# Kernel tuning notes

Hardware: AMD Instinct MI355X
Metric: run time of the kernel (lower is better)

## Reference

```python
import jax, jax.numpy as jnp
import numpy as np

H = 8
D_MODEL = 1024
DIM_G = 64
WAVE_LEN = 1000.0


def box_relational_embedding(f_g):
    # f_g: [B, N, 4] -> [B, N, N, 64] trigonometric geometry embedding
    B, N, _ = f_g.shape
    x_min, y_min, x_max, y_max = jnp.split(f_g, 4, axis=-1)  # each [B, N, 1]
    cx = (x_min + x_max) * 0.5
    cy = (y_min + y_max) * 0.5
    w = x_max - x_min + 1.0
    h = y_max - y_min + 1.0
    # row i vs column j deltas, normalized by row box size
    dx = jnp.log(jnp.maximum(jnp.abs((cx - cx.reshape(B, 1, N)) / w), 1e-3))
    dy = jnp.log(jnp.maximum(jnp.abs((cy - cy.reshape(B, 1, N)) / h), 1e-3))
    dw = jnp.log(w / w.reshape(B, 1, N))
    dh = jnp.log(h / h.reshape(B, 1, N))
    pos = jnp.stack([dx, dy, dw, dh], axis=-1)  # [B, N, N, 4]
    feat_range = jnp.arange(DIM_G // 8, dtype=jnp.float32) / (DIM_G / 8.0)
    dim_mat = 1.0 / jnp.power(WAVE_LEN, feat_range)  # [8]
    mul = (100.0 * pos)[..., None] * dim_mat  # [B, N, N, 4, 8]
    mul = mul.reshape(B, N, N, DIM_G // 2)
    return jnp.concatenate([jnp.sin(mul), jnp.cos(mul)], axis=-1)  # [B, N, N, 64]


def setup_inputs() -> dict:
    key = jax.random.key(0)
    ks = jax.random.split(key, 12)
    B, N, D = 16, 256, D_MODEL
    q = jax.random.normal(ks[0], (B, N, D), jnp.float32)
    k = jax.random.normal(ks[1], (B, N, D), jnp.float32)
    v = jax.random.normal(ks[2], (B, N, D), jnp.float32)
    # valid boxes: x_max > x_min, y_max > y_min
    xy = jax.random.uniform(ks[3], (B, N, 2), jnp.float32) * 100.0
    wh = jax.random.uniform(ks[4], (B, N, 2), jnp.float32) * 50.0 + 1.0
    input_box = jnp.concatenate([xy, xy + wh], axis=-1)  # [B, N, 4]
    s = 0.02
    Wq = jax.random.normal(ks[5], (D, D), jnp.float32) * s
    Wk = jax.random.normal(ks[6], (D, D), jnp.float32) * s
    Wv = jax.random.normal(ks[7], (D, D), jnp.float32) * s
    Wo = jax.random.normal(ks[8], (D, D), jnp.float32) * s
    bq = jnp.zeros((D,), jnp.float32)
    bk = jnp.zeros((D,), jnp.float32)
    bv = jnp.zeros((D,), jnp.float32)
    bo = jnp.zeros((D,), jnp.float32)
    Wg = jax.random.normal(ks[9], (H, DIM_G), jnp.float32) * 0.1  # stacked per-head Linear(64,1)
    bg = jax.random.normal(ks[10], (H,), jnp.float32) * 0.1
    return {"input_query": q, "input_key": k, "input_value": v, "input_box": input_box,
            "Wq": Wq, "bq": bq, "Wk": Wk, "bk": bk, "Wv": Wv, "bv": bv,
            "Wg": Wg, "bg": bg, "Wo": Wo, "bo": bo}


def reference(input_query, input_key, input_value, input_box,
              Wq, bq, Wk, bk, Wv, bv, Wg, bg, Wo, bo):
    B, N, D = input_query.shape
    d_k = D // H

    def proj(x, W, b):
        return (x @ W + b).reshape(B, N, H, d_k).transpose(0, 2, 1, 3)  # [B,H,N,dk]

    q = proj(input_query, Wq, bq)
    k = proj(input_key, Wk, bk)
    v = proj(input_value, Wv, bv)

    emb = box_relational_embedding(input_box)  # [B, N, N, 64]
    # per-head Linear(64 -> 1), stacked: [B, H, N, N]
    rel_w = jax.nn.relu(jnp.einsum('bmng,hg->bhmn', emb, Wg) + bg[None, :, None, None])

    scores = jnp.einsum('bhqd,bhkd->bhqk', q, k) / np.sqrt(d_k).astype(np.float32)
    logits = jnp.log(jnp.maximum(rel_w, 1e-6)) + scores
    attn = jax.nn.softmax(logits, axis=-1)  # [B, H, N, N]
    out = jnp.einsum('bhqk,bhkd->bhqd', attn, v)
    out = out.transpose(0, 2, 1, 3).reshape(B, N, D)
    return out @ Wo + bo
```

## Files before the change

kernel.cpp:

```cpp
#include <hip/hip_runtime.h>
#include <hip/hip_bf16.h>
#include <math.h>

#define B_  16
#define N_  256
#define D_  1024
#define H_  8
#define DK_ 128

typedef unsigned short u16;
typedef __attribute__((ext_vector_type(8))) short s8v;
typedef __attribute__((ext_vector_type(4))) float f4v;

__device__ __forceinline__ u16 f2b(float x) {
    union { float f; unsigned u; } v; v.f = x;
    unsigned r = v.u + 0x7fffu + ((v.u >> 16) & 1u);
    return (u16)(r >> 16);
}

__device__ __forceinline__ void gload16(void* lds, const void* g) {
    __builtin_amdgcn_global_load_lds(
        (const __attribute__((address_space(1))) void*)g,
        (__attribute__((address_space(3))) void*)lds, 16, 0, 0);
}

__global__ __launch_bounds__(256)
void cvt_kernel(const float* __restrict__ x0, const float* __restrict__ x1,
                const float* __restrict__ x2, u16* __restrict__ out)
{
    const float* in = (blockIdx.y == 0) ? x0 : (blockIdx.y == 1) ? x1 : x2;
    u16* o = out + (size_t)blockIdx.y * 4194304;
    const int i = blockIdx.x * 256 + threadIdx.x;
    const float4 a = ((const float4*)in)[2 * i];
    const float4 b = ((const float4*)in)[2 * i + 1];
    union { u16 s[8]; uint4 v; } t;
    t.s[0] = f2b(a.x); t.s[1] = f2b(a.y); t.s[2] = f2b(a.z); t.s[3] = f2b(a.w);
    t.s[4] = f2b(b.x); t.s[5] = f2b(b.y); t.s[6] = f2b(b.z); t.s[7] = f2b(b.w);
    ((uint4*)o)[i] = t.v;
}

__global__ __launch_bounds__(256)
void cvtT_kernel(const float* __restrict__ W0, const float* __restrict__ W1,
                 const float* __restrict__ W2, const float* __restrict__ W3,
                 u16* __restrict__ out)
{
    const float* W = (blockIdx.z == 0) ? W0 : (blockIdx.z == 1) ? W1 :
                     (blockIdx.z == 2) ? W2 : W3;
    u16* o = out + (size_t)blockIdx.z * (D_ * D_);
    __shared__ float t[32][33];
    const int k0 = blockIdx.x * 32, n0 = blockIdx.y * 32;
    const int c = threadIdx.x & 31, r8 = threadIdx.x >> 5;
#pragma unroll
    for (int rr = 0; rr < 4; ++rr)
        t[r8 + rr * 8][c] = W[(size_t)(k0 + r8 + rr * 8) * D_ + n0 + c];
    __syncthreads();
#pragma unroll
    for (int rr = 0; rr < 4; ++rr)
        o[(size_t)(n0 + r8 + rr * 8) * D_ + k0 + c] = f2b(t[c][r8 + rr * 8]);
}

__global__ __launch_bounds__(256)
void gemm_kernel(const u16* __restrict__ A0, const u16* __restrict__ Wt0,
                 const float* __restrict__ b0, const float* __restrict__ b1,
                 const float* __restrict__ b2, void* __restrict__ outb,
                 int mode)
{
    __shared__ __align__(16) u16 As[128][32];
    __shared__ __align__(16) u16 Bs[128][32];

    const int z = blockIdx.z;
    const u16* A  = A0  + (size_t)z * 4194304;
    const u16* Wt = Wt0 + (size_t)z * 1048576;
    const float* bias = (z == 0) ? b0 : (z == 1) ? b1 : b2;

    const int bid = blockIdx.x;
    const int xcd = bid & 7;
    const int wic = bid >> 3;
    const int by  = xcd * 4 + (wic & 3);
    const int bx  = wic >> 2;
    const int m0  = by * 128;
    const int n0  = bx * 128;

    const int tid  = threadIdx.x;
    const int lane = tid & 63;
    const int w    = tid >> 6;
    const int l15  = lane & 15;
    const int l4   = lane >> 4;
    const int wr   = w >> 1;
    const int wc   = w & 1;

    const int gr = tid >> 2;
    const int gc = (tid & 3) * 8;
    const u16* asrc = A  + (size_t)(m0 + gr) * 1024 + gc;
    const u16* bsrc = Wt + (size_t)(n0 + gr) * 1024 + gc;

    f4v acc[4][4] = {};

    for (int kt = 0; kt < 32; ++kt) {
        const int k0 = kt * 32;
        __syncthreads();
        gload16(&As[gr][gc],      asrc + k0);
        gload16(&As[64 + gr][gc], asrc + 64 * 1024 + k0);
        gload16(&Bs[gr][gc],      bsrc + k0);
        gload16(&Bs[64 + gr][gc], bsrc + 64 * 1024 + k0);
        __syncthreads();

        s8v af[4], bf[4];
#pragma unroll
        for (int i = 0; i < 4; ++i)
            af[i] = *(const s8v*)&As[wr * 64 + i * 16 + l15][l4 * 8];
#pragma unroll
        for (int j = 0; j < 4; ++j)
            bf[j] = *(const s8v*)&Bs[wc * 64 + j * 16 + l15][l4 * 8];
#pragma unroll
        for (int i = 0; i < 4; ++i)
#pragma unroll
            for (int j = 0; j < 4; ++j)
                acc[i][j] = __builtin_amdgcn_mfma_f32_16x16x32_bf16(
                    af[i], bf[j], acc[i][j], 0, 0, 0);
    }

#pragma unroll
    for (int j = 0; j < 4; ++j) {
        const int n = n0 + wc * 64 + j * 16 + l15;
        const float bb = bias[n];
#pragma unroll
        for (int i = 0; i < 4; ++i) {
#pragma unroll
            for (int reg = 0; reg < 4; ++reg) {
                const int m = m0 + wr * 64 + i * 16 + l4 * 4 + reg;
                const float val = acc[i][j][reg] + bb;
                if (mode == 0) {
                    ((float*)outb)[(size_t)m * 1024 + n] = val;
                } else {
                    const int b = m >> 8, tok = m & 255;
                    const int h = n >> 7, d = n & 127;
                    ((u16*)outb)[(size_t)z * 4194304 +
                                 (((size_t)b * H_ + h) * N_ + tok) * DK_ + d] = f2b(val);
                }
            }
        }
    }
}

__global__ __launch_bounds__(256)
void boxbias_kernel(const float* __restrict__ fg, const float* __restrict__ Wg,
                    const float* __restrict__ bg, float* __restrict__ lb)
{
    __shared__ float sWg[512];
    __shared__ float sbg[8];
    const int tid = threadIdx.x;
    const int b = blockIdx.x >> 8;
    const int i = blockIdx.x & 255;

    sWg[tid] = Wg[tid];
    sWg[tid + 256] = Wg[tid + 256];
    if (tid < 8) sbg[tid] = bg[tid];

    const float4 bi = *(const float4*)&fg[(size_t)(b * N_ + i) * 4];
    const float cxi = 0.5f * (bi.x + bi.z);
    const float cyi = 0.5f * (bi.y + bi.w);
    const float wi  = bi.z - bi.x + 1.0f;
    const float hi  = bi.w - bi.y + 1.0f;

    const int j = tid;
    const float4 bj = *(const float4*)&fg[(size_t)(b * N_ + j) * 4];
    const float cxj = 0.5f * (bj.x + bj.z);
    const float cyj = 0.5f * (bj.y + bj.w);
    const float wj  = bj.z - bj.x + 1.0f;
    const float hj  = bj.w - bj.y + 1.0f;

    const float pos[4] = {
        logf(fmaxf(fabsf((cxi - cxj) / wi), 1e-3f)) * 100.0f,
        logf(fmaxf(fabsf((cyi - cyj) / hi), 1e-3f)) * 100.0f,
        logf(wi / wj) * 100.0f,
        logf(hi / hj) * 100.0f
    };
    const float dim[8] = {1.0f, 0.421696503f, 0.177827941f, 0.0749894209f,
                          0.0316227766f, 0.0133352143f, 0.00562341325f, 0.00237137371f};

    float sv[32], cv[32];
#pragma unroll
    for (int p = 0; p < 4; ++p)
#pragma unroll
        for (int q = 0; q < 8; ++q)
            __sincosf(pos[p] * dim[q], &sv[p * 8 + q], &cv[p * 8 + q]);

    __syncthreads();
#pragma unroll
    for (int h = 0; h < 8; ++h) {
        float acc = sbg[h];
        const float* wrow = &sWg[h * 64];
#pragma unroll
        for (int g = 0; g < 32; ++g)
            acc = fmaf(sv[g], wrow[g], fmaf(cv[g], wrow[32 + g], acc));
        const float rel = fmaxf(acc, 0.0f);
        lb[(((size_t)b * H_ + h) * N_ + i) * N_ + j] = logf(fmaxf(rel, 1e-6f));
    }
}

__global__ __launch_bounds__(256)
void attn_mfma_kernel(const u16* __restrict__ qp, const u16* __restrict__ kp,
                      const u16* __restrict__ vp, const float* __restrict__ lb,
                      u16* __restrict__ ao)
{
    __shared__ __align__(16) u16 Ks[32][136];
    __shared__ __align__(16) u16 Vt[128][40];
    __shared__ __align__(16) u16 Ps[4][32][40];

    const int tid  = threadIdx.x;
    const int lane = tid & 63;
    const int w    = tid >> 6;
    const int l15  = lane & 15;
    const int l4   = lane >> 4;
    const int bh   = blockIdx.x >> 1;
    const int qt   = blockIdx.x & 1;
    const int q0   = qt * 128 + w * 32;

    s8v qf[2][4];
    const u16* qb = qp + ((size_t)bh * N_ + q0) * DK_;
#pragma unroll
    for (int mf = 0; mf < 2; ++mf)
#pragma unroll
        for (int ks = 0; ks < 4; ++ks)
            qf[mf][ks] = *(const s8v*)(qb + (size_t)(mf * 16 + l15) * DK_ + ks * 32 + l4 * 8);

    f4v o[2][8] = {};
    float m_r[2][4], l_r[2][4];
#pragma unroll
    for (int mf = 0; mf < 2; ++mf)
#pragma unroll
        for (int r = 0; r < 4; ++r) { m_r[mf][r] = -INFINITY; l_r[mf][r] = 0.0f; }

    const float scale = 0.08838834764831845f;
    const float* lbb = lb + ((size_t)bh * N_ + q0) * N_;

    const int sr = tid >> 3;
    const int sc = (tid & 7) * 16;

    for (int kt = 0; kt < 8; ++kt) {
        __syncthreads();
        {
            const u16* ksrc = kp + ((size_t)bh * N_ + kt * 32) * DK_;
            *(s8v*)&Ks[sr][sc]     = *(const s8v*)(ksrc + (size_t)sr * DK_ + sc);
            *(s8v*)&Ks[sr][sc + 8] = *(const s8v*)(ksrc + (size_t)sr * DK_ + sc + 8);
        }
        {
            const u16* vsrc = vp + ((size_t)bh * N_ + kt * 32) * DK_;
            const s8v v0 = *(const s8v*)(vsrc + (size_t)sr * DK_ + sc);
            const s8v v1 = *(const s8v*)(vsrc + (size_t)sr * DK_ + sc + 8);
#pragma unroll
            for (int jj = 0; jj < 8; ++jj) {
                Vt[sc + jj][sr]     = (u16)v0[jj];
                Vt[sc + 8 + jj][sr] = (u16)v1[jj];
            }
        }
        __syncthreads();

        f4v s[2][2] = {};
#pragma unroll
        for (int ks = 0; ks < 4; ++ks) {
#pragma unroll
            for (int kf = 0; kf < 2; ++kf) {
                const s8v kb = *(const s8v*)&Ks[kf * 16 + l15][ks * 32 + l4 * 8];
#pragma unroll
                for (int mf = 0; mf < 2; ++mf)
                    s[mf][kf] = __builtin_amdgcn_mfma_f32_16x16x32_bf16(
                        qf[mf][ks], kb, s[mf][kf], 0, 0, 0);
            }
        }
#pragma unroll
        for (int mf = 0; mf < 2; ++mf)
#pragma unroll
            for (int kf = 0; kf < 2; ++kf)
#pragma unroll
                for (int r = 0; r < 4; ++r)
                    s[mf][kf][r] = fmaf(s[mf][kf][r], scale,
                        lbb[(size_t)(mf * 16 + l4 * 4 + r) * N_ + kt * 32 + kf * 16 + l15]);

#pragma unroll
        for (int mf = 0; mf < 2; ++mf) {
            float rm[4], al[4];
#pragma unroll
            for (int r = 0; r < 4; ++r) rm[r] = fmaxf(s[mf][0][r], s[mf][1][r]);
#pragma unroll
            for (int st = 1; st <= 8; st <<= 1)
#pragma unroll
                for (int r = 0; r < 4; ++r) rm[r] = fmaxf(rm[r], __shfl_xor(rm[r], st));
#pragma unroll
            for (int r = 0; r < 4; ++r) {
                const float mn = fmaxf(m_r[mf][r], rm[r]);
                al[r] = __expf(m_r[mf][r] - mn);
                m_r[mf][r] = mn;
            }
            float p0[4], p1[4], rs[4];
#pragma unroll
            for (int r = 0; r < 4; ++r) {
                p0[r] = __expf(s[mf][0][r] - m_r[mf][r]);
                p1[r] = __expf(s[mf][1][r] - m_r[mf][r]);
                rs[r] = p0[r] + p1[r];
            }
#pragma unroll
            for (int st = 1; st <= 8; st <<= 1)
#pragma unroll
                for (int r = 0; r < 4; ++r) rs[r] += __shfl_xor(rs[r], st);
#pragma unroll
            for (int r = 0; r < 4; ++r) {
                l_r[mf][r] = l_r[mf][r] * al[r] + rs[r];
                Ps[w][mf * 16 + l4 * 4 + r][l15]      = f2b(p0[r]);
                Ps[w][mf * 16 + l4 * 4 + r][16 + l15] = f2b(p1[r]);
            }
#pragma unroll
            for (int nf = 0; nf < 8; ++nf)
#pragma unroll
                for (int r = 0; r < 4; ++r) o[mf][nf][r] *= al[r];
        }

        s8v pa[2];
#pragma unroll
        for (int mf = 0; mf < 2; ++mf)
            pa[mf] = *(const s8v*)&Ps[w][mf * 16 + l15][l4 * 8];
#pragma unroll
        for (int nf = 0; nf < 8; ++nf) {
            const s8v vb = *(const s8v*)&Vt[nf * 16 + l15][l4 * 8];
#pragma unroll
            for (int mf = 0; mf < 2; ++mf)
                o[mf][nf] = __builtin_amdgcn_mfma_f32_16x16x32_bf16(
                    pa[mf], vb, o[mf][nf], 0, 0, 0);
        }
    }

    const int b = bh >> 3, h = bh & 7;
#pragma unroll
    for (int mf = 0; mf < 2; ++mf) {
        float inv[4];
#pragma unroll
        for (int r = 0; r < 4; ++r) inv[r] = 1.0f / l_r[mf][r];
#pragma unroll
        for (int nf = 0; nf < 8; ++nf) {
#pragma unroll
            for (int r = 0; r < 4; ++r) {
                const int tok = q0 + mf * 16 + l4 * 4 + r;
                const int d = nf * 16 + l15;
                ao[(((size_t)b * N_ + tok) * H_ + h) * DK_ + d] = f2b(o[mf][nf][r] * inv[r]);
            }
        }
    }
}

extern "C" void kernel_launch(void* const* d_in, const int* in_sizes, int n_in,
                              void* d_out, int out_size, void* d_ws, size_t ws_size,
                              hipStream_t stream)
{
    const float* xq = (const float*)d_in[0];
    const float* xk = (const float*)d_in[1];
    const float* xv = (const float*)d_in[2];
    const float* fg = (const float*)d_in[3];
    const float* Wq = (const float*)d_in[4];
    const float* bq = (const float*)d_in[5];
    const float* Wk = (const float*)d_in[6];
    const float* bk = (const float*)d_in[7];
    const float* Wv = (const float*)d_in[8];
    const float* bv = (const float*)d_in[9];
    const float* Wg = (const float*)d_in[10];
    const float* bg = (const float*)d_in[11];
    const float* Wo = (const float*)d_in[12];
    const float* bo = (const float*)d_in[13];

    char* w8 = (char*)d_ws;
    u16*   xb  = (u16*)(w8);
    u16*   Wt  = (u16*)(w8 + 25165824);
    u16*   qkv = (u16*)(w8 + 33554432);
    float* lb  = (float*)(w8 + 58720256);
    u16*   ao  = (u16*)(w8 + 92274688);

    cvt_kernel<<<dim3(2048, 3), 256, 0, stream>>>(xq, xk, xv, xb);
    cvtT_kernel<<<dim3(32, 32, 4), 256, 0, stream>>>(Wq, Wk, Wv, Wo, Wt);

    gemm_kernel<<<dim3(256, 1, 3), 256, 0, stream>>>(xb, Wt, bq, bk, bv, qkv, 1);

    boxbias_kernel<<<B_ * N_, 256, 0, stream>>>(fg, Wg, bg, lb);

    attn_mfma_kernel<<<B_ * H_ * 2, 256, 0, stream>>>(
        qkv, qkv + 4194304, qkv + 2 * 4194304, lb, ao);

    gemm_kernel<<<dim3(256, 1, 1), 256, 0, stream>>>(
        ao, Wt + 3 * 1048576, bo, bo, bo, d_out, 0);
}
```

Before: 149.1 us.

## Double-buffer GEMM with swizzled LDS, store V transposed, fp16 log-bias

The GEMM now double-buffers its LDS tiles and prefetches the next K slice while the current one runs MFMA, with an XOR swizzle on the LDS columns to cut bank conflicts. The V projection is written out already transposed ([d][tok]) with vector stores, so the attention kernel loads Vt with vector copies instead of scalar transposing writes. The log relational bias buffer is stored as fp16, halving its write and read traffic. The fp16 bias adds precision loss, and the extra LDS buffer doubles the GEMM's shared memory.

```diff
diff --git a/kernel.cpp b/kernel.cpp
--- a/kernel.cpp
+++ b/kernel.cpp
@@ -1,5 +1,6 @@
 #include <hip/hip_runtime.h>
 #include <hip/hip_bf16.h>
+#include <hip/hip_fp16.h>
 #include <math.h>
 
 #define B_  16
@@ -65,8 +66,8 @@
                  const float* __restrict__ b2, void* __restrict__ outb,
                  int mode)
 {
-    __shared__ __align__(16) u16 As[128][32];
-    __shared__ __align__(16) u16 Bs[128][32];
+    __shared__ __align__(16) u16 As[2][128][32];
+    __shared__ __align__(16) u16 Bs[2][128][32];
 
     const int z = blockIdx.z;
     const u16* A  = A0  + (size_t)z * 4194304;
@@ -89,36 +90,50 @@
     const int wr   = w >> 1;
     const int wc   = w & 1;
 
-    const int gr = tid >> 2;
-    const int gc = (tid & 3) * 8;
-    const u16* asrc = A  + (size_t)(m0 + gr) * 1024 + gc;
-    const u16* bsrc = Wt + (size_t)(n0 + gr) * 1024 + gc;
+    const int gr   = tid >> 2;
+    const int c4   = tid & 3;
+    const int sw   = (gr >> 1) & 3;
+    const int scol = (c4 ^ sw) * 8;
+    const int doff = c4 * 8;
+    const u16* asrc = A  + (size_t)(m0 + gr) * 1024 + scol;
+    const u16* bsrc = Wt + (size_t)(n0 + gr) * 1024 + scol;
+
+    const int fc = (l4 ^ ((l15 >> 1) & 3)) * 8;
 
     f4v acc[4][4] = {};
 
+#define STAGE(buf, kt) do { \
+        const int k0_ = (kt) * 32; \
+        gload16(&As[buf][gr][doff],      asrc + k0_); \
+        gload16(&As[buf][gr + 64][doff], asrc + 64 * 1024 + k0_); \
+        gload16(&Bs[buf][gr][doff],      bsrc + k0_); \
+        gload16(&Bs[buf][gr + 64][doff], bsrc + 64 * 1024 + k0_); \
+    } while (0)
+
+    STAGE(0, 0);
+    __syncthreads();
+
     for (int kt = 0; kt < 32; ++kt) {
-        const int k0 = kt * 32;
-        __syncthreads();
-        gload16(&As[gr][gc],      asrc + k0);
-        gload16(&As[64 + gr][gc], asrc + 64 * 1024 + k0);
-        gload16(&Bs[gr][gc],      bsrc + k0);
-        gload16(&Bs[64 + gr][gc], bsrc + 64 * 1024 + k0);
-        __syncthreads();
+        const int cur = kt & 1;
+        if (kt < 31) STAGE(cur ^ 1, kt + 1);
 
         s8v af[4], bf[4];
 #pragma unroll
         for (int i = 0; i < 4; ++i)
-            af[i] = *(const s8v*)&As[wr * 64 + i * 16 + l15][l4 * 8];
+            af[i] = *(const s8v*)&As[cur][wr * 64 + i * 16 + l15][fc];
 #pragma unroll
         for (int j = 0; j < 4; ++j)
-            bf[j] = *(const s8v*)&Bs[wc * 64 + j * 16 + l15][l4 * 8];
+            bf[j] = *(const s8v*)&Bs[cur][wc * 64 + j * 16 + l15][fc];
 #pragma unroll
         for (int i = 0; i < 4; ++i)
 #pragma unroll
             for (int j = 0; j < 4; ++j)
                 acc[i][j] = __builtin_amdgcn_mfma_f32_16x16x32_bf16(
                     af[i], bf[j], acc[i][j], 0, 0, 0);
+
+        __syncthreads();
     }
+#undef STAGE
 
 #pragma unroll
     for (int j = 0; j < 4; ++j) {
@@ -126,17 +141,31 @@
         const float bb = bias[n];
 #pragma unroll
         for (int i = 0; i < 4; ++i) {
-#pragma unroll
-            for (int reg = 0; reg < 4; ++reg) {
-                const int m = m0 + wr * 64 + i * 16 + l4 * 4 + reg;
-                const float val = acc[i][j][reg] + bb;
-                if (mode == 0) {
-                    ((float*)outb)[(size_t)m * 1024 + n] = val;
-                } else {
+            const int mbase = m0 + wr * 64 + i * 16 + l4 * 4;
+            if (mode == 0) {
+#pragma unroll
+                for (int reg = 0; reg < 4; ++reg)
+                    ((float*)outb)[(size_t)(mbase + reg) * 1024 + n] =
+                        acc[i][j][reg] + bb;
+            } else if (z == 2) {
+                const int b = mbase >> 8, tok = mbase & 255;
+                const int h = n >> 7, d = n & 127;
+                ushort4 st;
+                st.x = f2b(acc[i][j][0] + bb);
+                st.y = f2b(acc[i][j][1] + bb);
+                st.z = f2b(acc[i][j][2] + bb);
+                st.w = f2b(acc[i][j][3] + bb);
+                *(ushort4*)&((u16*)outb)[(size_t)z * 4194304 +
+                    (((size_t)b * H_ + h) * DK_ + d) * N_ + tok] = st;
+            } else {
+                const int h = n >> 7, d = n & 127;
+#pragma unroll
+                for (int reg = 0; reg < 4; ++reg) {
+                    const int m = mbase + reg;
                     const int b = m >> 8, tok = m & 255;
-                    const int h = n >> 7, d = n & 127;
                     ((u16*)outb)[(size_t)z * 4194304 +
-                                 (((size_t)b * H_ + h) * N_ + tok) * DK_ + d] = f2b(val);
+                        (((size_t)b * H_ + h) * N_ + tok) * DK_ + d] =
+                        f2b(acc[i][j][reg] + bb);
                 }
             }
         }
@@ -145,7 +174,7 @@
 
 __global__ __launch_bounds__(256)
 void boxbias_kernel(const float* __restrict__ fg, const float* __restrict__ Wg,
-                    const float* __restrict__ bg, float* __restrict__ lb)
+                    const float* __restrict__ bg, _Float16* __restrict__ lb)
 {
     __shared__ float sWg[512];
     __shared__ float sbg[8];
@@ -195,13 +224,14 @@
         for (int g = 0; g < 32; ++g)
             acc = fmaf(sv[g], wrow[g], fmaf(cv[g], wrow[32 + g], acc));
         const float rel = fmaxf(acc, 0.0f);
-        lb[(((size_t)b * H_ + h) * N_ + i) * N_ + j] = logf(fmaxf(rel, 1e-6f));
+        lb[(((size_t)b * H_ + h) * N_ + i) * N_ + j] =
+            (_Float16)logf(fmaxf(rel, 1e-6f));
     }
 }
 
 __global__ __launch_bounds__(256)
 void attn_mfma_kernel(const u16* __restrict__ qp, const u16* __restrict__ kp,
-                      const u16* __restrict__ vp, const float* __restrict__ lb,
+                      const u16* __restrict__ vp, const _Float16* __restrict__ lb,
                       u16* __restrict__ ao)
 {
     __shared__ __align__(16) u16 Ks[32][136];
@@ -233,10 +263,12 @@
         for (int r = 0; r < 4; ++r) { m_r[mf][r] = -INFINITY; l_r[mf][r] = 0.0f; }
 
     const float scale = 0.08838834764831845f;
-    const float* lbb = lb + ((size_t)bh * N_ + q0) * N_;
+    const _Float16* lbb = lb + ((size_t)bh * N_ + q0) * N_;
 
     const int sr = tid >> 3;
     const int sc = (tid & 7) * 16;
+    const int vr = tid >> 2;
+    const int vs = (tid & 3) * 8;
 
     for (int kt = 0; kt < 8; ++kt) {
         __syncthreads();
@@ -246,14 +278,11 @@
             *(s8v*)&Ks[sr][sc + 8] = *(const s8v*)(ksrc + (size_t)sr * DK_ + sc + 8);
         }
         {
-            const u16* vsrc = vp + ((size_t)bh * N_ + kt * 32) * DK_;
-            const s8v v0 = *(const s8v*)(vsrc + (size_t)sr * DK_ + sc);
-            const s8v v1 = *(const s8v*)(vsrc + (size_t)sr * DK_ + sc + 8);
-#pragma unroll
-            for (int jj = 0; jj < 8; ++jj) {
-                Vt[sc + jj][sr]     = (u16)v0[jj];
-                Vt[sc + 8 + jj][sr] = (u16)v1[jj];
-            }
+            const u16* vsrc = vp + ((size_t)bh * DK_ + vr) * N_ + kt * 32 + vs;
+            const s8v v0 = *(const s8v*)vsrc;
+            const s8v v1 = *(const s8v*)(vsrc + 64 * N_);
+            *(s8v*)&Vt[vr][vs]      = v0;
+            *(s8v*)&Vt[vr + 64][vs] = v1;
         }
         __syncthreads();
 
@@ -275,7 +304,7 @@
             for (int kf = 0; kf < 2; ++kf)
 #pragma unroll
                 for (int r = 0; r < 4; ++r)
-                    s[mf][kf][r] = fmaf(s[mf][kf][r], scale,
+                    s[mf][kf][r] = fmaf(s[mf][kf][r], scale, (float)
                         lbb[(size_t)(mf * 16 + l4 * 4 + r) * N_ + kt * 32 + kf * 16 + l15]);
 
 #pragma unroll
@@ -368,11 +397,11 @@
     const float* bo = (const float*)d_in[13];
 
     char* w8 = (char*)d_ws;
-    u16*   xb  = (u16*)(w8);
-    u16*   Wt  = (u16*)(w8 + 25165824);
-    u16*   qkv = (u16*)(w8 + 33554432);
-    float* lb  = (float*)(w8 + 58720256);
-    u16*   ao  = (u16*)(w8 + 92274688);
+    u16*      xb  = (u16*)(w8);
+    u16*      Wt  = (u16*)(w8 + 25165824);
+    u16*      qkv = (u16*)(w8 + 33554432);
+    _Float16* lb  = (_Float16*)(w8 + 58720256);
+    u16*      ao  = (u16*)(w8 + 75497472);
 
     cvt_kernel<<<dim3(2048, 3), 256, 0, stream>>>(xq, xk, xv, xb);
     cvtT_kernel<<<dim3(32, 32, 4), 256, 0, stream>>>(Wq, Wk, Wv, Wo, Wt);
```

Measured after the change: 138.7 us. -6.9%, faster.
